# Performance work log

Hardware: AMD Instinct MI355X
Metric: run time of the kernel (lower is better)

The kernel has to match this reference:

```python
import jax, jax.numpy as jnp
import numpy as np

N = 10000    # nodes
D = 128      # d_model
K = 16       # d_state
S = 5        # seq_len (tokens per node)
E = 320000   # edges
R = 200      # num relation types
P = E // (S - 1)  # edges sampled per tokenizer step
EPS = 1e-5


def setup_inputs() -> dict:
    key = jax.random.key(0)
    ks = jax.random.split(key, 16)
    sc = 1.0 / np.sqrt(D)
    return {
        "x": jax.random.normal(ks[0], (N, D), jnp.float32),
        "edge_index": jax.random.randint(ks[1], (2, E), 0, N),
        "edge_type": jax.random.randint(ks[2], (E,), 0, R),
        "perms": jax.random.randint(ks[3], (S - 1, P), 0, E),
        "rel_table": jax.random.normal(ks[4], (R, D), jnp.float32) * 0.1,
        "log_A": jax.random.normal(ks[5], (D, K), jnp.float32) * 0.1,
        "W_B": jax.random.normal(ks[6], (D, K), jnp.float32) * sc,
        "W_C": jax.random.normal(ks[7], (D, K), jnp.float32) * sc,
        "W_delta": jax.random.normal(ks[8], (D, D), jnp.float32) * sc,
        "b_delta": jnp.zeros((D,), jnp.float32),
        "W_g": jax.random.normal(ks[9], (D, D), jnp.float32) * sc,
        "b_g": jnp.zeros((D,), jnp.float32),
        "W_out": jax.random.normal(ks[10], (D, D), jnp.float32) * sc,
        "b_out": jnp.zeros((D,), jnp.float32),
        "ln_g": jnp.ones((D,), jnp.float32),
        "ln_b": jnp.zeros((D,), jnp.float32),
    }


def _tokenize(x, edge_index, edge_type, perms, rel_table):
    # x: [N,D]; perms: [S-1,P] -> tokens [N,S,D]
    src, dst = edge_index[0], edge_index[1]
    step_src = src[perms]                    # [S-1,P]
    step_dst = dst[perms]                    # [S-1,P]
    msg = x[step_src] + rel_table[edge_type[perms]]  # [S-1,P,D]
    seg = jax.vmap(lambda i, m: jax.ops.segment_sum(m, i, num_segments=N))(step_dst, msg)  # [S-1,N,D]
    deg = jax.vmap(lambda i: jax.ops.segment_sum(jnp.ones((P,), x.dtype), i, num_segments=N))(step_dst)  # [S-1,N]
    neigh = seg / jnp.clip(deg, 1.0)[..., None]
    return jnp.concatenate([x[:, None, :], jnp.moveaxis(neigh, 0, 1)], axis=1)  # [N,S,D]


def _selective_scan(tokens, log_A, W_B, W_C, W_delta, b_delta):
    # tokens: [N,S,D] -> [N,S,D]
    deltas = jax.nn.softplus(tokens @ W_delta + b_delta)  # [N,S,D]
    Bs = tokens @ W_B                                     # [N,S,K]
    Cs = tokens @ W_C                                     # [N,S,K]
    A_cont = -jnp.exp(log_A)                              # [D,K]
    A_disc = jnp.exp(deltas[..., None] * A_cont)          # [N,S,D,K]
    Bx = deltas[..., None] * Bs[:, :, None, :] * tokens[..., None]  # [N,S,D,K] = B_disc * x_k

    def step(state, xs):
        a, bx, c = xs                          # [N,D,K],[N,D,K],[N,K]
        state = a * state + bx
        y = jnp.einsum('ndk,nk->nd', state, c)
        return state, y

    init = jnp.zeros((tokens.shape[0], D, K), tokens.dtype)
    _, ys = jax.lax.scan(step, init, (jnp.moveaxis(A_disc, 1, 0),
                                      jnp.moveaxis(Bx, 1, 0),
                                      jnp.moveaxis(Cs, 1, 0)))
    return jnp.moveaxis(ys, 0, 1)  # [N,S,D]


def reference(x, edge_index, edge_type, perms, rel_table, log_A, W_B, W_C,
              W_delta, b_delta, W_g, b_g, W_out, b_out, ln_g, ln_b):
    tokens = _tokenize(x, edge_index, edge_type, perms, rel_table)
    out_f = _selective_scan(tokens, log_A, W_B, W_C, W_delta, b_delta)
    out_b = _selective_scan(tokens[:, ::-1, :], log_A, W_B, W_C, W_delta, b_delta)
    scan_out = (out_f + out_b[:, ::-1, :]).mean(axis=1)  # [N,D]
    gate = jax.nn.silu(x @ W_g + b_g)
    res = x + gate * (scan_out @ W_out + b_out)
    mu = res.mean(axis=-1, keepdims=True)
    var = res.var(axis=-1, keepdims=True)
    return (res - mu) / jnp.sqrt(var + EPS) * ln_g + ln_b
```

## Files before the change

kernel.cpp:

```cpp
#include <hip/hip_runtime.h>
#include <hip/hip_bf16.h>
#include <math.h>

#define N_NODES 10000
#define D_MODEL 128
#define E_EDGES 320000
#define P_EDGES 80000
#define LN_EPS 1e-5f
#define NBUCK 40960
#define CAP 32
#define M_ROWS 50000
#define M_PAD  50048
#define NPAD   320

typedef __attribute__((ext_vector_type(8))) short bf16x8;
typedef __attribute__((ext_vector_type(4))) float f32x4;

__device__ __forceinline__ unsigned short f2bf(float f) {
    __hip_bfloat16 h = __float2bfloat16(f);
    return *reinterpret_cast<unsigned short*>(&h);
}
__device__ __forceinline__ float bf2f(unsigned int u) {
    return __uint_as_float(u << 16);
}

__global__ __launch_bounds__(256) void prep_all(
    const float* __restrict__ Wd, const float* __restrict__ Wb,
    const float* __restrict__ Wc, const float* __restrict__ Wg,
    const float* __restrict__ W_out,
    const float* __restrict__ x, const float* __restrict__ rel,
    const int* __restrict__ edge_index, const int* __restrict__ edge_type,
    unsigned short* __restrict__ Bp, unsigned short* __restrict__ Wop,
    unsigned short* __restrict__ x_bf, unsigned short* __restrict__ rel_bf,
    int* __restrict__ cnt, int4* __restrict__ ed4,
    unsigned short* __restrict__ tokens)
{
    int gid = blockIdx.x * 256 + threadIdx.x;
    if (gid < 40960) {
        int k = gid / NPAD, n = gid - (gid / NPAD) * NPAD;
        float v = 0.f;
        if (n < 128)      v = Wd[k * 128 + n];
        else if (n < 144) v = Wb[k * 16 + (n - 128)];
        else if (n < 160) v = Wc[k * 16 + (n - 144)];
        else if (n < 288) v = Wg[k * 128 + (n - 160)];
        Bp[((size_t)(k >> 3) * NPAD + n) * 8 + (k & 7)] = f2bf(v);
    } else if (gid < 57344) {
        int i = gid - 40960;
        int k = i >> 7, n = i & 127;
        Wop[((size_t)(k >> 3) * 128 + n) * 8 + (k & 7)] = f2bf(W_out[k * 128 + n]);
    } else if (gid < 98304) {
        cnt[gid - 57344] = 0;
    } else if (gid < 123904) {
        int i = gid - 98304;
        rel_bf[i] = f2bf(rel[i]);
    } else if (gid < 1403904) {
        int i = gid - 123904;
        unsigned short v = f2bf(x[i]);
        x_bf[i] = v;
        tokens[(size_t)(i >> 7) * 640 + (i & 127)] = v;
    } else if (gid < 1723904) {
        int e = gid - 1403904;
        ed4[e] = make_int4(edge_index[e], edge_index[E_EDGES + e], edge_type[e], 0);
    }
}

__global__ __launch_bounds__(256) void csr_build(
    const int4* __restrict__ ed4, const int* __restrict__ perms,
    int* __restrict__ cnt, int2* __restrict__ slots)
{
    int gid = blockIdx.x * blockDim.x + threadIdx.x;
    if (gid >= 4 * P_EDGES) return;
    int s = gid / P_EDGES;
    int e = perms[gid];
    int4 ed = ed4[e];
    int b = ed.y * 4 + s;
    int pos = atomicAdd(&cnt[b], 1);
    if (pos < CAP) slots[(size_t)b * CAP + pos] = make_int2(ed.x, ed.z);
}

__global__ __launch_bounds__(256) void gather_tokens(
    const unsigned short* __restrict__ x_bf,
    const int* __restrict__ cnt, const int2* __restrict__ slots,
    const unsigned short* __restrict__ rel_bf,
    unsigned short* __restrict__ tokens)
{
    int n = blockIdx.x;
    int w = threadIdx.x >> 6, lane = threadIdx.x & 63;
    int b = n * 4 + w;
    int c = cnt[b];
    int cc = c < CAP ? c : CAP;
    const int2* sl = slots + (size_t)b * CAP;
    const unsigned int* xu = (const unsigned int*)x_bf;
    const unsigned int* ru = (const unsigned int*)rel_bf;
    float ax = 0.f, ay = 0.f;
    int j = 0;
    for (; j + 4 <= cc; j += 4) {
        int4 e01 = *(const int4*)(sl + j);
        int4 e23 = *(const int4*)(sl + j + 2);
        unsigned int x0 = xu[(size_t)e01.x * 64 + lane];
        unsigned int r0 = ru[(size_t)e01.y * 64 + lane];
        unsigned int x1 = xu[(size_t)e01.z * 64 + lane];
        unsigned int r1 = ru[(size_t)e01.w * 64 + lane];
        unsigned int x2 = xu[(size_t)e23.x * 64 + lane];
        unsigned int r2 = ru[(size_t)e23.y * 64 + lane];
        unsigned int x3 = xu[(size_t)e23.z * 64 + lane];
        unsigned int r3 = ru[(size_t)e23.w * 64 + lane];
        ax += (bf2f(x0 & 0xffffu) + bf2f(r0 & 0xffffu))
            + (bf2f(x1 & 0xffffu) + bf2f(r1 & 0xffffu))
            + (bf2f(x2 & 0xffffu) + bf2f(r2 & 0xffffu))
            + (bf2f(x3 & 0xffffu) + bf2f(r3 & 0xffffu));
        ay += (bf2f(x0 >> 16) + bf2f(r0 >> 16))
            + (bf2f(x1 >> 16) + bf2f(r1 >> 16))
            + (bf2f(x2 >> 16) + bf2f(r2 >> 16))
            + (bf2f(x3 >> 16) + bf2f(r3 >> 16));
    }
    if (j + 2 <= cc) {
        int4 e01 = *(const int4*)(sl + j);
        unsigned int x0 = xu[(size_t)e01.x * 64 + lane];
        unsigned int r0 = ru[(size_t)e01.y * 64 + lane];
        unsigned int x1 = xu[(size_t)e01.z * 64 + lane];
        unsigned int r1 = ru[(size_t)e01.w * 64 + lane];
        ax += (bf2f(x0 & 0xffffu) + bf2f(r0 & 0xffffu))
            + (bf2f(x1 & 0xffffu) + bf2f(r1 & 0xffffu));
        ay += (bf2f(x0 >> 16) + bf2f(r0 >> 16))
            + (bf2f(x1 >> 16) + bf2f(r1 >> 16));
        j += 2;
    }
    if (j < cc) {
        int2 se = sl[j];
        unsigned int xa = xu[(size_t)se.x * 64 + lane];
        unsigned int ra = ru[(size_t)se.y * 64 + lane];
        ax += bf2f(xa & 0xffffu) + bf2f(ra & 0xffffu);
        ay += bf2f(xa >> 16) + bf2f(ra >> 16);
    }
    float inv = 1.f / fmaxf((float)c, 1.f);
    unsigned int pack = (unsigned int)f2bf(ax * inv)
                      | ((unsigned int)f2bf(ay * inv) << 16);
    ((unsigned int*)tokens)[((size_t)n * 5 + w + 1) * 64 + lane] = pack;
}

__global__ __launch_bounds__(256) void mfma_gemm(
    const unsigned short* __restrict__ tokens,
    const unsigned short* __restrict__ Bp,
    const float* __restrict__ b_delta, const float* __restrict__ b_g,
    unsigned short* __restrict__ delta,
    unsigned short* __restrict__ bc,
    unsigned short* __restrict__ g)
{
    int m0 = blockIdx.x * 64, n0 = blockIdx.y * 64;
    int wv = threadIdx.x >> 6, lane = threadIdx.x & 63;
    int quad = lane >> 4, l16 = lane & 15;

    f32x4 acc[4] = {{0,0,0,0},{0,0,0,0},{0,0,0,0},{0,0,0,0}};
    const unsigned short* arow = tokens + (size_t)(m0 + wv * 16 + l16) * 128 + quad * 8;
    #pragma unroll
    for (int kc = 0; kc < 128; kc += 32) {
        bf16x8 a = *(const bf16x8*)(arow + kc);
        #pragma unroll
        for (int t = 0; t < 4; ++t) {
            bf16x8 b = *(const bf16x8*)(Bp + ((size_t)(kc / 8 + quad) * NPAD + n0 + 16 * t + l16) * 8);
            acc[t] = __builtin_amdgcn_mfma_f32_16x16x32_bf16(a, b, acc[t], 0, 0, 0);
        }
    }

    int rbase = m0 + wv * 16 + quad * 4;
    #pragma unroll
    for (int t = 0; t < 4; ++t) {
        int c = n0 + 16 * t + l16;
        #pragma unroll
        for (int reg = 0; reg < 4; ++reg) {
            int r = rbase + reg;
            if (r >= M_ROWS) continue;
            float v = acc[t][reg];
            if (c < 128) {
                float z = v + b_delta[c];
                float d = (z > 15.f) ? z : log1pf(__expf(z));
                delta[(size_t)r * 128 + c] = f2bf(d);
            } else if (c < 160) {
                bc[(size_t)r * 32 + (c - 128)] = f2bf(v);
            } else if (c < 288) {
                int rq = r / 5;
                if (r - rq * 5 == 0)
                    g[(size_t)rq * 128 + (c - 160)] = f2bf(v + b_g[c - 160]);
            }
        }
    }
}

#define SOS 136
__global__ __launch_bounds__(256) void scan_out(
    const unsigned short* __restrict__ tokens,
    const unsigned short* __restrict__ delta,
    const unsigned short* __restrict__ bcbuf,
    const float* __restrict__ log_A,
    const unsigned short* __restrict__ Wop,
    const unsigned short* __restrict__ gbuf,
    const float* __restrict__ x,
    const float* __restrict__ b_out,
    const float* __restrict__ ln_g, const float* __restrict__ ln_b,
    float* __restrict__ out)
{
    const int m0 = blockIdx.x * 16;
    const int t = threadIdx.x;
    const int wv = t >> 6, lane = t & 63;
    const int quad = lane >> 4, l16 = lane & 15;

    __shared__ __align__(16) float BCs[16][160];
    __shared__ __align__(16) unsigned short soL[16][SOS];
    __shared__ float res[16][132];
    __shared__ float pmu[16][16], pv2[16][16];
    __shared__ float muA[16], rstdA[16];

    for (int idx = t; idx < 2560; idx += 256) {
        int n = idx / 160, rem = idx - n * 160;
        int s = rem >> 5, q = rem & 31;
        BCs[n][rem] = bf2f(bcbuf[((size_t)(m0 + n) * 5 + s) * 32 + q]);
    }

    const int d = t & 127;
    float Ac[16];
    {
        const float4* la = (const float4*)(log_A + d * 16);
        #pragma unroll
        for (int q = 0; q < 4; ++q) {
            float4 lv = la[q];
            Ac[q * 4 + 0] = -__expf(lv.x);
            Ac[q * 4 + 1] = -__expf(lv.y);
            Ac[q * 4 + 2] = -__expf(lv.z);
            Ac[q * 4 + 3] = -__expf(lv.w);
        }
    }
    __syncthreads();

    #pragma unroll 1
    for (int i = 0; i < 8; ++i) {
        int nl = 2 * i + (t >> 7);
        const unsigned short* tb = tokens + ((size_t)(m0 + nl) * 5) * 128 + d;
        const unsigned short* db = delta  + ((size_t)(m0 + nl) * 5) * 128 + d;
        float tv[5], dl[5];
        #pragma unroll
        for (int s = 0; s < 5; ++s) {
            tv[s] = bf2f(tb[s * 128]);
            dl[s] = bf2f(db[s * 128]);
        }
        const float* BCn = &BCs[nl][0];

        float st[16], V[16];
        #pragma unroll
        for (int k = 0; k < 16; ++k) { st[k] = 0.f; V[k] = BCn[16 + k]; }
        float total = 0.f;
        #pragma unroll
        for (int s = 0; s < 5; ++s) {
            float dtv = dl[s] * tv[s];
            float yf = 0.f, ub = 0.f;
            #pragma unroll
            for (int k = 0; k < 16; ++k) {
                float B = BCn[s * 32 + k];
                float C = BCn[s * 32 + 16 + k];
                float A = __expf(dl[s] * Ac[k]);
                st[k] = fmaf(A, st[k], dtv * B);
                yf = fmaf(st[k], C, yf);
                ub = fmaf(V[k], B, ub);
                if (s < 4) V[k] = fmaf(A, V[k], BCn[(s + 1) * 32 + 16 + k]);
            }
            total += yf + dtv * ub;
        }
        soL[nl][d] = f2bf(total * 0.2f);
    }
    __syncthreads();

    f32x4 acc[2] = {{0,0,0,0},{0,0,0,0}};
    #pragma unroll
    for (int kc = 0; kc < 4; ++kc) {
        bf16x8 a = *(const bf16x8*)&soL[l16][kc * 32 + quad * 8];
        #pragma unroll
        for (int tt = 0; tt < 2; ++tt) {
            int tc = wv * 2 + tt;
            bf16x8 b = *(const bf16x8*)(Wop + ((size_t)(kc * 4 + quad) * 128 + 16 * tc + l16) * 8);
            acc[tt] = __builtin_amdgcn_mfma_f32_16x16x32_bf16(a, b, acc[tt], 0, 0, 0);
        }
    }
    #pragma unroll
    for (int tt = 0; tt < 2; ++tt) {
        int c = wv * 32 + tt * 16 + l16;
        #pragma unroll
        for (int reg = 0; reg < 4; ++reg) {
            int lrow = quad * 4 + reg;
            float o = acc[tt][reg] + b_out[c];
            float gl = bf2f(gbuf[(size_t)(m0 + lrow) * 128 + c]);
            float gate = gl / (1.f + __expf(-gl));
            res[lrow][c] = x[(size_t)(m0 + lrow) * 128 + c] + gate * o;
        }
    }
    __syncthreads();

    {
        int row = t >> 4, q = t & 15;
        float s = 0.f, s2 = 0.f;
        #pragma unroll
        for (int i = 0; i < 8; ++i) {
            float v = res[row][q + 16 * i];
            s += v; s2 += v * v;
        }
        pmu[row][q] = s; pv2[row][q] = s2;
    }
    __syncthreads();
    if (t < 16) {
        float s = 0.f, s2 = 0.f;
        #pragma unroll
        for (int i = 0; i < 16; ++i) { s += pmu[t][i]; s2 += pv2[t][i]; }
        float mu = s * (1.f / 128.f);
        float var = s2 * (1.f / 128.f) - mu * mu;
        muA[t] = mu;
        rstdA[t] = rsqrtf(var + LN_EPS);
    }
    __syncthreads();
    #pragma unroll
    for (int i = 0; i < 8; ++i) {
        int idx = i * 256 + t;
        int row = idx >> 7, c = idx & 127;
        out[(size_t)(m0 + row) * 128 + c] =
            (res[row][c] - muA[row]) * rstdA[row] * ln_g[c] + ln_b[c];
    }
}

extern "C" void kernel_launch(void* const* d_in, const int* in_sizes, int n_in,
                              void* d_out, int out_size, void* d_ws, size_t ws_size,
                              hipStream_t stream) {
    const float* x          = (const float*)d_in[0];
    const int*   edge_index = (const int*)  d_in[1];
    const int*   edge_type  = (const int*)  d_in[2];
    const int*   perms      = (const int*)  d_in[3];
    const float* rel_table  = (const float*)d_in[4];
    const float* log_A      = (const float*)d_in[5];
    const float* W_B        = (const float*)d_in[6];
    const float* W_C        = (const float*)d_in[7];
    const float* W_delta    = (const float*)d_in[8];
    const float* b_delta    = (const float*)d_in[9];
    const float* W_g        = (const float*)d_in[10];
    const float* b_g        = (const float*)d_in[11];
    const float* W_out      = (const float*)d_in[12];
    const float* b_out      = (const float*)d_in[13];
    const float* ln_g       = (const float*)d_in[14];
    const float* ln_b       = (const float*)d_in[15];

    char* ws = (char*)d_ws;
    int*            cnt    = (int*)           (ws + 0);
    unsigned short* Bp     = (unsigned short*)(ws + 163840);
    unsigned short* Wop    = (unsigned short*)(ws + 245760);
    unsigned short* x_bf   = (unsigned short*)(ws + 278528);
    unsigned short* rel_bf = (unsigned short*)(ws + 2838528);
    int4*           ed4    = (int4*)          (ws + 2889728);
    unsigned short* tokens = (unsigned short*)(ws + 8009728);
    unsigned short* g      = (unsigned short*)(ws + 20822016);
    unsigned short* bc     = (unsigned short*)(ws + 23382016);
    int2*           slots  = (int2*)          (ws + 26582016);
    unsigned short* delta  = (unsigned short*)(ws + 26582016);

    prep_all<<<(1723904 + 255) / 256, 256, 0, stream>>>(
        W_delta, W_B, W_C, W_g, W_out, x, rel_table, edge_index, edge_type,
        Bp, Wop, x_bf, rel_bf, cnt, ed4, tokens);

    csr_build<<<(4 * P_EDGES + 255) / 256, 256, 0, stream>>>(
        ed4, perms, cnt, slots);

    gather_tokens<<<N_NODES, 256, 0, stream>>>(
        x_bf, cnt, slots, rel_bf, tokens);

    mfma_gemm<<<dim3(M_PAD / 64, NPAD / 64), 256, 0, stream>>>(
        tokens, Bp, b_delta, b_g, delta, bc, g);

    scan_out<<<N_NODES / 16, 256, 0, stream>>>(
        tokens, delta, bc, log_A, Wop, g, x, b_out, ln_g, ln_b, (float*)d_out);
}
```

Measured before the change: 219.4 us.

## Split fused scan+output kernel into per-node scan and separate output GEMM

```diff
diff --git a/kernel.cpp b/kernel.cpp
--- a/kernel.cpp
+++ b/kernel.cpp
@@ -187,12 +187,68 @@
     }
 }
 
-#define SOS 136
-__global__ __launch_bounds__(256) void scan_out(
+__global__ __launch_bounds__(128) void scan_so(
     const unsigned short* __restrict__ tokens,
     const unsigned short* __restrict__ delta,
     const unsigned short* __restrict__ bcbuf,
     const float* __restrict__ log_A,
+    unsigned short* __restrict__ so)
+{
+    const int n = blockIdx.x, t = threadIdx.x;
+    __shared__ __align__(16) float BC[160];
+
+    for (int idx = t; idx < 160; idx += 128)
+        BC[idx] = bf2f(bcbuf[(size_t)n * 160 + idx]);
+
+    float tv[5], dl[5];
+    {
+        const unsigned short* tb = tokens + (size_t)n * 640 + t;
+        const unsigned short* db = delta  + (size_t)n * 640 + t;
+        #pragma unroll
+        for (int s = 0; s < 5; ++s) {
+            tv[s] = bf2f(tb[s * 128]);
+            dl[s] = bf2f(db[s * 128]);
+        }
+    }
+    float Ac[16];
+    {
+        const float4* la = (const float4*)(log_A + t * 16);
+        #pragma unroll
+        for (int q = 0; q < 4; ++q) {
+            float4 lv = la[q];
+            Ac[q * 4 + 0] = -__expf(lv.x);
+            Ac[q * 4 + 1] = -__expf(lv.y);
+            Ac[q * 4 + 2] = -__expf(lv.z);
+            Ac[q * 4 + 3] = -__expf(lv.w);
+        }
+    }
+    __syncthreads();
+
+    float st[16], V[16];
+    #pragma unroll
+    for (int k = 0; k < 16; ++k) { st[k] = 0.f; V[k] = BC[16 + k]; }
+    float total = 0.f;
+    #pragma unroll
+    for (int s = 0; s < 5; ++s) {
+        float dtv = dl[s] * tv[s];
+        float yf = 0.f, ub = 0.f;
+        #pragma unroll
+        for (int k = 0; k < 16; ++k) {
+            float B = BC[s * 32 + k];
+            float C = BC[s * 32 + 16 + k];
+            float A = __expf(dl[s] * Ac[k]);
+            st[k] = fmaf(A, st[k], dtv * B);
+            yf = fmaf(st[k], C, yf);
+            ub = fmaf(V[k], B, ub);
+            if (s < 4) V[k] = fmaf(A, V[k], BC[(s + 1) * 32 + 16 + k]);
+        }
+        total += yf + dtv * ub;
+    }
+    so[(size_t)n * 128 + t] = f2bf(total * 0.2f);
+}
+
+__global__ __launch_bounds__(256) void out_gemm(
+    const unsigned short* __restrict__ so,
     const unsigned short* __restrict__ Wop,
     const unsigned short* __restrict__ gbuf,
     const float* __restrict__ x,
@@ -200,127 +256,71 @@
     const float* __restrict__ ln_g, const float* __restrict__ ln_b,
     float* __restrict__ out)
 {
-    const int m0 = blockIdx.x * 16;
-    const int t = threadIdx.x;
-    const int wv = t >> 6, lane = t & 63;
-    const int quad = lane >> 4, l16 = lane & 15;
-
-    __shared__ __align__(16) float BCs[16][160];
-    __shared__ __align__(16) unsigned short soL[16][SOS];
-    __shared__ float res[16][132];
-    __shared__ float pmu[16][16], pv2[16][16];
+    int m0 = blockIdx.x * 16;
+    int tid = threadIdx.x;
+    int wv = tid >> 6, lane = tid & 63;
+    int quad = lane >> 4, l16 = lane & 15;
+
+    __shared__ float res[16 * 132];
+    __shared__ float pmu[16][16];
+    __shared__ float pv2[16][16];
     __shared__ float muA[16], rstdA[16];
 
-    for (int idx = t; idx < 2560; idx += 256) {
-        int n = idx / 160, rem = idx - n * 160;
-        int s = rem >> 5, q = rem & 31;
-        BCs[n][rem] = bf2f(bcbuf[((size_t)(m0 + n) * 5 + s) * 32 + q]);
-    }
-
-    const int d = t & 127;
-    float Ac[16];
-    {
-        const float4* la = (const float4*)(log_A + d * 16);
-        #pragma unroll
-        for (int q = 0; q < 4; ++q) {
-            float4 lv = la[q];
-            Ac[q * 4 + 0] = -__expf(lv.x);
-            Ac[q * 4 + 1] = -__expf(lv.y);
-            Ac[q * 4 + 2] = -__expf(lv.z);
-            Ac[q * 4 + 3] = -__expf(lv.w);
-        }
-    }
-    __syncthreads();
-
-    #pragma unroll 1
-    for (int i = 0; i < 8; ++i) {
-        int nl = 2 * i + (t >> 7);
-        const unsigned short* tb = tokens + ((size_t)(m0 + nl) * 5) * 128 + d;
-        const unsigned short* db = delta  + ((size_t)(m0 + nl) * 5) * 128 + d;
-        float tv[5], dl[5];
-        #pragma unroll
-        for (int s = 0; s < 5; ++s) {
-            tv[s] = bf2f(tb[s * 128]);
-            dl[s] = bf2f(db[s * 128]);
-        }
-        const float* BCn = &BCs[nl][0];
-
-        float st[16], V[16];
-        #pragma unroll
-        for (int k = 0; k < 16; ++k) { st[k] = 0.f; V[k] = BCn[16 + k]; }
-        float total = 0.f;
-        #pragma unroll
-        for (int s = 0; s < 5; ++s) {
-            float dtv = dl[s] * tv[s];
-            float yf = 0.f, ub = 0.f;
-            #pragma unroll
-            for (int k = 0; k < 16; ++k) {
-                float B = BCn[s * 32 + k];
-                float C = BCn[s * 32 + 16 + k];
-                float A = __expf(dl[s] * Ac[k]);
-                st[k] = fmaf(A, st[k], dtv * B);
-                yf = fmaf(st[k], C, yf);
-                ub = fmaf(V[k], B, ub);
-                if (s < 4) V[k] = fmaf(A, V[k], BCn[(s + 1) * 32 + 16 + k]);
-            }
-            total += yf + dtv * ub;
-        }
-        soL[nl][d] = f2bf(total * 0.2f);
-    }
-    __syncthreads();
-
     f32x4 acc[2] = {{0,0,0,0},{0,0,0,0}};
-    #pragma unroll
-    for (int kc = 0; kc < 4; ++kc) {
-        bf16x8 a = *(const bf16x8*)&soL[l16][kc * 32 + quad * 8];
+    const unsigned short* arow = so + (size_t)(m0 + l16) * 128 + quad * 8;
+    #pragma unroll
+    for (int kc = 0; kc < 128; kc += 32) {
+        bf16x8 a = *(const bf16x8*)(arow + kc);
         #pragma unroll
         for (int tt = 0; tt < 2; ++tt) {
-            int tc = wv * 2 + tt;
-            bf16x8 b = *(const bf16x8*)(Wop + ((size_t)(kc * 4 + quad) * 128 + 16 * tc + l16) * 8);
+            int t = wv * 2 + tt;
+            bf16x8 b = *(const bf16x8*)(Wop + ((size_t)(kc / 8 + quad) * 128 + 16 * t + l16) * 8);
             acc[tt] = __builtin_amdgcn_mfma_f32_16x16x32_bf16(a, b, acc[tt], 0, 0, 0);
         }
     }
+
     #pragma unroll
     for (int tt = 0; tt < 2; ++tt) {
         int c = wv * 32 + tt * 16 + l16;
         #pragma unroll
         for (int reg = 0; reg < 4; ++reg) {
             int lrow = quad * 4 + reg;
+            int r = m0 + lrow;
             float o = acc[tt][reg] + b_out[c];
-            float gl = bf2f(gbuf[(size_t)(m0 + lrow) * 128 + c]);
+            float gl = bf2f(gbuf[(size_t)r * 128 + c]);
             float gate = gl / (1.f + __expf(-gl));
-            res[lrow][c] = x[(size_t)(m0 + lrow) * 128 + c] + gate * o;
+            res[lrow * 132 + c] = x[(size_t)r * 128 + c] + gate * o;
         }
     }
     __syncthreads();
 
     {
-        int row = t >> 4, q = t & 15;
+        int row = tid >> 4, q = tid & 15;
         float s = 0.f, s2 = 0.f;
         #pragma unroll
         for (int i = 0; i < 8; ++i) {
-            float v = res[row][q + 16 * i];
+            float v = res[row * 132 + q + 16 * i];
             s += v; s2 += v * v;
         }
         pmu[row][q] = s; pv2[row][q] = s2;
     }
     __syncthreads();
-    if (t < 16) {
+    if (tid < 16) {
         float s = 0.f, s2 = 0.f;
         #pragma unroll
-        for (int i = 0; i < 16; ++i) { s += pmu[t][i]; s2 += pv2[t][i]; }
+        for (int i = 0; i < 16; ++i) { s += pmu[tid][i]; s2 += pv2[tid][i]; }
         float mu = s * (1.f / 128.f);
         float var = s2 * (1.f / 128.f) - mu * mu;
-        muA[t] = mu;
-        rstdA[t] = rsqrtf(var + LN_EPS);
+        muA[tid] = mu;
+        rstdA[tid] = rsqrtf(var + LN_EPS);
     }
     __syncthreads();
     #pragma unroll
     for (int i = 0; i < 8; ++i) {
-        int idx = i * 256 + t;
+        int idx = i * 256 + tid;
         int row = idx >> 7, c = idx & 127;
         out[(size_t)(m0 + row) * 128 + c] =
-            (res[row][c] - muA[row]) * rstdA[row] * ln_g[c] + ln_b[c];
+            (res[row * 132 + c] - muA[row]) * rstdA[row] * ln_g[c] + ln_b[c];
     }
 }
 
@@ -356,6 +356,7 @@
     unsigned short* bc     = (unsigned short*)(ws + 23382016);
     int2*           slots  = (int2*)          (ws + 26582016);
     unsigned short* delta  = (unsigned short*)(ws + 26582016);
+    unsigned short* so     = (unsigned short*)(ws + 39394304);
 
     prep_all<<<(1723904 + 255) / 256, 256, 0, stream>>>(
         W_delta, W_B, W_C, W_g, W_out, x, rel_table, edge_index, edge_type,
@@ -370,6 +371,9 @@
     mfma_gemm<<<dim3(M_PAD / 64, NPAD / 64), 256, 0, stream>>>(
         tokens, Bp, b_delta, b_g, delta, bc, g);
 
-    scan_out<<<N_NODES / 16, 256, 0, stream>>>(
-        tokens, delta, bc, log_A, Wop, g, x, b_out, ln_g, ln_b, (float*)d_out);
-}
+    scan_so<<<N_NODES, 128, 0, stream>>>(
+        tokens, delta, bc, log_A, so);
+
+    out_gemm<<<N_NODES / 16, 256, 0, stream>>>(
+        so, Wop, g, x, b_out, ln_g, ln_b, (float*)d_out);
+}
```

New measurement: 198.9 us, median of 2. 9.3% less time.
